# Kernel optimization log

Measured on AMD Instinct MI355X. Metric: run time of the kernel, lower is better.

Reference implementation:

```python
import jax, jax.numpy as jnp
import numpy as np

N = 10000
E = 160000
D_IN = 512
D_OUT = 512


def setup_inputs() -> dict:
    key = jax.random.key(0)
    k1, k2, k3, k4, k5 = jax.random.split(key, 5)
    x = jax.random.normal(k1, (N, D_IN), dtype=jnp.float32)
    edge_index = jax.random.randint(k2, (2, E), 0, N, dtype=jnp.int64)
    edge_attr = jax.random.uniform(k3, (E,), dtype=jnp.float32)
    W = jax.random.normal(k4, (D_IN, D_OUT), dtype=jnp.float32) * 0.05
    b = jax.random.normal(k5, (D_OUT,), dtype=jnp.float32) * 0.05
    return {"x": x, "edge_index": edge_index, "edge_attr": edge_attr, "W": W, "b": b}


def reference(x, edge_index, edge_attr, W, b):
    # PyG GCNConv with normalize=True, add_self_loops=True, edge_weight=edge_attr.
    n = x.shape[0]
    row, col = edge_index[0], edge_index[1]
    # Add self loops with weight 1.0 (fill_value=1.)
    loop = jnp.arange(n, dtype=edge_index.dtype)
    row_f = jnp.concatenate([row, loop])      # [E+N] source nodes
    col_f = jnp.concatenate([col, loop])      # [E+N] target nodes
    ew = jnp.concatenate([edge_attr, jnp.ones((n,), dtype=edge_attr.dtype)])
    # Symmetric normalization: deg computed over target index (col)
    deg = jax.ops.segment_sum(ew, col_f, num_segments=n)
    dinv = jnp.where(deg > 0, jax.lax.rsqrt(deg), 0.0)
    norm = dinv[row_f] * ew * dinv[col_f]     # [E+N]
    # Linear transform (no bias inside lin), then gather-scale-scatter
    h = x @ W                                  # [N, D_OUT]
    msg = h[row_f] * norm[:, None]             # [E+N, D_OUT]
    out = jax.ops.segment_sum(msg, col_f, num_segments=n)
    return out + b
```

## Files before the change

### kernel.cpp

```cpp
#include <hip/hip_runtime.h>

#define NN 10000
#define EE 160000
#define DD 512
#define CAP 128

typedef float floatx4 __attribute__((ext_vector_type(4)));
typedef short short8 __attribute__((ext_vector_type(8)));

#define AS3(p) ((__attribute__((address_space(3))) void*)(p))
#define AS1(p) ((const __attribute__((address_space(1))) void*)(p))

static __device__ __forceinline__ unsigned short f2bf(float f) {
    unsigned int u = __float_as_uint(f);
    unsigned int r = (u + 0x7fffu + ((u >> 16) & 1u)) >> 16;
    return (unsigned short)r;
}
static __device__ __forceinline__ float bflo(unsigned int u) {
    return __uint_as_float(u << 16);
}
static __device__ __forceinline__ float bfhi(unsigned int u) {
    return __uint_as_float(u & 0xffff0000u);
}


#define WT_BLOCKS 256
#define ZERO_BLOCKS 20
#define EDGE_BLOCKS 625
#define GM_BLOCKS (157 * 4)

__global__ __launch_bounds__(256) void k_prep_w(const float* __restrict__ W,
                                                unsigned short* __restrict__ wtb,
                                                uint4* __restrict__ zbase) {
    const int b = blockIdx.x;
    const int tid = threadIdx.x;
    if (b < WT_BLOCKS) {
        __shared__ float T[32][33];
        int bi = b & 15;
        int bj = b >> 4;
        int r0 = tid >> 5;
        int cc = tid & 31;
        #pragma unroll
        for (int k = 0; k < 4; k++) {
            int r = r0 + k * 8;
            T[r][cc] = W[(size_t)(bi * 32 + r) * DD + bj * 32 + cc];
        }
        __syncthreads();
        #pragma unroll
        for (int k = 0; k < 4; k++) {
            int r = r0 + k * 8;
            wtb[(size_t)(bj * 32 + r) * DD + bi * 32 + cc] = f2bf(T[cc][r]);
        }
    } else {
        int idx = (b - WT_BLOCKS) * 256 + tid;
        zbase[idx] = make_uint4(0u, 0u, 0u, 0u);
    }
}


__global__ __launch_bounds__(256) void k_gemm_edge(const float* __restrict__ x,
                                                   const unsigned short* __restrict__ wtb,
                                                   unsigned short* __restrict__ hb,
                                                   const int* __restrict__ row,
                                                   const int* __restrict__ col,
                                                   const float* __restrict__ ew,
                                                   float* __restrict__ deg,
                                                   int* __restrict__ cursor,
                                                   uint2* __restrict__ erw) {
    __shared__ unsigned short As[64 * 32];
    __shared__ unsigned short Bs[128 * 32];

    const int tid = threadIdx.x;

    if (blockIdx.x < EDGE_BLOCKS) {
        int e = blockIdx.x * 256 + tid;
        int r = row[e];
        int t = col[e];
        float w = ew[e];
        atomicAdd(&deg[t], w);
        int p = atomicAdd(&cursor[t], 1);
        if (p < CAP) erw[t * CAP + p] = make_uint2((unsigned int)r, __float_as_uint(w));
        return;
    }

    const int bid = blockIdx.x - EDGE_BLOCKS;
    const int wave = tid >> 6;
    const int lane = tid & 63;

    const int bm = (bid >> 2) * 64;
    const int bn = (bid & 3) * 128;

    const int wm = (wave >> 1) * 32;
    const int wn = (wave & 1) * 64;

    const int fm = lane & 15;
    const int kb = (lane >> 4) * 8;

    floatx4 acc[2][4];
    #pragma unroll
    for (int i = 0; i < 2; i++)
        #pragma unroll
        for (int j = 0; j < 4; j++)
            acc[i][j] = (floatx4){0.f, 0.f, 0.f, 0.f};

    const int srow = lane >> 2;
    const int scol = (lane & 3) * 8;

    int gr = bm + wave * 16 + srow; if (gr > NN - 1) gr = NN - 1;
    const float* xrow = x + (size_t)gr * DD + scol;

    for (int k0 = 0; k0 < DD; k0 += 32) {
        {
            float4 v0 = *(const float4*)(xrow + k0);
            float4 v1 = *(const float4*)(xrow + k0 + 4);
            unsigned int u0 = (unsigned int)f2bf(v0.x) | ((unsigned int)f2bf(v0.y) << 16);
            unsigned int u1 = (unsigned int)f2bf(v0.z) | ((unsigned int)f2bf(v0.w) << 16);
            unsigned int u2 = (unsigned int)f2bf(v1.x) | ((unsigned int)f2bf(v1.y) << 16);
            unsigned int u3 = (unsigned int)f2bf(v1.z) | ((unsigned int)f2bf(v1.w) << 16);
            *(uint4*)&As[(size_t)(wave * 16 + srow) * 32 + scol] = make_uint4(u0, u1, u2, u3);
        }
        #pragma unroll
        for (int cc = 0; cc < 2; cc++) {
            int c = wave + cc * 4;
            int nr = bn + c * 16 + srow;
            __builtin_amdgcn_global_load_lds(AS1(wtb + (size_t)nr * DD + k0 + scol),
                                             AS3(&Bs[c * 512]), 16, 0, 0);
        }
        __syncthreads();

        short8 af[2], bfr[4];
        #pragma unroll
        for (int mi = 0; mi < 2; mi++)
            af[mi] = *(const short8*)&As[(wm + mi * 16 + fm) * 32 + kb];
        #pragma unroll
        for (int ni = 0; ni < 4; ni++)
            bfr[ni] = *(const short8*)&Bs[(wn + ni * 16 + fm) * 32 + kb];

        #pragma unroll
        for (int mi = 0; mi < 2; mi++)
            #pragma unroll
            for (int ni = 0; ni < 4; ni++)
                acc[mi][ni] = __builtin_amdgcn_mfma_f32_16x16x32_bf16(af[mi], bfr[ni], acc[mi][ni], 0, 0, 0);

        __syncthreads();
    }

    #pragma unroll
    for (int mi = 0; mi < 2; mi++) {
        #pragma unroll
        for (int ni = 0; ni < 4; ni++) {
            int colg = bn + wn + ni * 16 + (lane & 15);
            int rbase = bm + wm + mi * 16 + (lane >> 4) * 4;
            #pragma unroll
            for (int j = 0; j < 4; j++) {
                int rg = rbase + j;
                if (rg < NN) hb[(size_t)rg * DD + colg] = f2bf(acc[mi][ni][j]);
            }
        }
    }
}


#define EDGE_FMA(P, W) a0 += bflo(P) * W; a1 += bfhi(P) * W;

__global__ __launch_bounds__(128, 8) void k_aggregate(const int* __restrict__ cursor,
                                                      const uint2* __restrict__ erw,
                                                      const unsigned short* __restrict__ hb,
                                                      const float* __restrict__ deg,
                                                      const float* __restrict__ bias,
                                                      float* __restrict__ out) {
    const int h = threadIdx.x >> 6;
    const int t = threadIdx.x & 63;
    const int bid = blockIdx.x;
    const int q = bid & 3;
    const int i = (bid >> 2) * 2 + h;
    const int c = q * 128 + t * 2;

    __shared__ int   s_r[2][CAP];
    __shared__ float s_w[2][CAP];

    int cnt = cursor[i];
    if (cnt > CAP) cnt = CAP;
    const uint2* bkt = erw + (size_t)i * CAP;
    if (t < cnt) {
        uint2 p = bkt[t];
        int r = (int)p.x;
        s_r[h][t] = r << 9;
        s_w[h][t] = __uint_as_float(p.y) * rsqrtf(deg[r] + 1.0f);
    }
    if (t + 64 < cnt) {
        uint2 p = bkt[t + 64];
        int r = (int)p.x;
        s_r[h][t + 64] = r << 9;
        s_w[h][t + 64] = __uint_as_float(p.y) * rsqrtf(deg[r] + 1.0f);
    }

    float dv = rsqrtf(deg[i] + 1.0f);
    unsigned int hv = *(const unsigned int*)&hb[(size_t)i * DD + c];
    float2 bv = *(const float2*)&bias[c];

    __syncthreads();

    float a0 = 0.f, a1 = 0.f;

    int j = 0;
    for (; j + 8 <= cnt; j += 8) {
        unsigned int p0 = *(const unsigned int*)&hb[s_r[h][j    ] + c];
        unsigned int p1 = *(const unsigned int*)&hb[s_r[h][j + 1] + c];
        unsigned int p2 = *(const unsigned int*)&hb[s_r[h][j + 2] + c];
        unsigned int p3 = *(const unsigned int*)&hb[s_r[h][j + 3] + c];
        unsigned int p4 = *(const unsigned int*)&hb[s_r[h][j + 4] + c];
        unsigned int p5 = *(const unsigned int*)&hb[s_r[h][j + 5] + c];
        unsigned int p6 = *(const unsigned int*)&hb[s_r[h][j + 6] + c];
        unsigned int p7 = *(const unsigned int*)&hb[s_r[h][j + 7] + c];
        float w0 = s_w[h][j],     w1 = s_w[h][j + 1], w2 = s_w[h][j + 2], w3 = s_w[h][j + 3];
        float w4 = s_w[h][j + 4], w5 = s_w[h][j + 5], w6 = s_w[h][j + 6], w7 = s_w[h][j + 7];
        EDGE_FMA(p0, w0) EDGE_FMA(p1, w1) EDGE_FMA(p2, w2) EDGE_FMA(p3, w3)
        EDGE_FMA(p4, w4) EDGE_FMA(p5, w5) EDGE_FMA(p6, w6) EDGE_FMA(p7, w7)
    }
    for (; j + 4 <= cnt; j += 4) {
        unsigned int p0 = *(const unsigned int*)&hb[s_r[h][j    ] + c];
        unsigned int p1 = *(const unsigned int*)&hb[s_r[h][j + 1] + c];
        unsigned int p2 = *(const unsigned int*)&hb[s_r[h][j + 2] + c];
        unsigned int p3 = *(const unsigned int*)&hb[s_r[h][j + 3] + c];
        float w0 = s_w[h][j], w1 = s_w[h][j + 1], w2 = s_w[h][j + 2], w3 = s_w[h][j + 3];
        EDGE_FMA(p0, w0) EDGE_FMA(p1, w1) EDGE_FMA(p2, w2) EDGE_FMA(p3, w3)
    }
    for (; j < cnt; j++) {
        unsigned int p0 = *(const unsigned int*)&hb[s_r[h][j] + c];
        float w0 = s_w[h][j];
        EDGE_FMA(p0, w0)
    }

    float2 o;
    o.x = (a0 + bflo(hv) * dv) * dv + bv.x;
    o.y = (a1 + bfhi(hv) * dv) * dv + bv.y;
    *(float2*)&out[(size_t)i * DD + c] = o;
}

extern "C" void kernel_launch(void* const* d_in, const int* in_sizes, int n_in,
                              void* d_out, int out_size, void* d_ws, size_t ws_size,
                              hipStream_t stream) {
    const float* x  = (const float*)d_in[0];
    const int*   ei = (const int*)d_in[1];
    const float* ea = (const float*)d_in[2];
    const float* W  = (const float*)d_in[3];
    const float* b  = (const float*)d_in[4];
    float* out = (float*)d_out;

    char* ws = (char*)d_ws;
    unsigned short* hb   = (unsigned short*)ws;
    unsigned short* wtb  = (unsigned short*)(ws + 20480000);
    float* deg    = (float*)(ws + 21004288);
    int*   cursor = (int*)  (ws + 21045248);
    uint2* erw    = (uint2*)(ws + 21086208);

    const int* row = ei;
    const int* col = ei + EE;

    k_prep_w<<<WT_BLOCKS + ZERO_BLOCKS, 256, 0, stream>>>(W, wtb, (uint4*)deg);

    k_gemm_edge<<<EDGE_BLOCKS + GM_BLOCKS, 256, 0, stream>>>(x, wtb, hb, row, col, ea,
                                                             deg, cursor, erw);

    k_aggregate<<<NN * 2, 128, 0, stream>>>(cursor, erw, hb, deg, b, out);
}
```

Before: 129.0 us.

## Pre-convert x to bf16 and double-buffer GEMM LDS loads via global_load_lds

Adds a separate pass that converts x to bf16 with a packed convert instruction. The GEMM can then stream both A and B tiles straight into LDS with global_load_lds. The GEMM loop becomes double-buffered with one barrier per k-step, so the next tile loads while the MFMAs run on the current one. Degree and cursor zeroing moves from extra kernel blocks to a hipMemsetAsync. In exchange, the conversion pass writes and re-reads a 10 MB bf16 copy of x and adds a memset call on the stream.

New measurement: 132.0 us. 1.02x slower.

```diff
diff --git a/kernel.cpp b/kernel.cpp
--- a/kernel.cpp
+++ b/kernel.cpp
@@ -16,6 +16,11 @@
     unsigned int r = (u + 0x7fffu + ((u >> 16) & 1u)) >> 16;
     return (unsigned short)r;
 }
+static __device__ __forceinline__ unsigned int cvtpk(float a, float b) {
+    unsigned int r;
+    asm("v_cvt_pk_bf16_f32 %0, %1, %2" : "=v"(r) : "v"(a), "v"(b));
+    return r;
+}
 static __device__ __forceinline__ float bflo(unsigned int u) {
     return __uint_as_float(u << 16);
 }
@@ -24,20 +29,26 @@
 }
 
 
+#define XB_BLOCKS 5000
 #define WT_BLOCKS 256
-#define ZERO_BLOCKS 20
-#define EDGE_BLOCKS 625
+#define EDGE_BLOCKS 632
 #define GM_BLOCKS (157 * 4)
 
-__global__ __launch_bounds__(256) void k_prep_w(const float* __restrict__ W,
-                                                unsigned short* __restrict__ wtb,
-                                                uint4* __restrict__ zbase) {
+__global__ __launch_bounds__(256) void k_prep_xw(const float* __restrict__ x,
+                                                 const float* __restrict__ W,
+                                                 unsigned short* __restrict__ xb,
+                                                 unsigned short* __restrict__ wtb) {
     const int b = blockIdx.x;
     const int tid = threadIdx.x;
-    if (b < WT_BLOCKS) {
+    if (b < XB_BLOCKS) {
+        int gid = b * 256 + tid;
+        float4 v = *(const float4*)&x[(size_t)gid * 4];
+        *(uint2*)&xb[(size_t)gid * 4] = make_uint2(cvtpk(v.x, v.y), cvtpk(v.z, v.w));
+    } else {
         __shared__ float T[32][33];
-        int bi = b & 15;
-        int bj = b >> 4;
+        int idx = b - XB_BLOCKS;
+        int bi = idx & 15;
+        int bj = idx >> 4;
         int r0 = tid >> 5;
         int cc = tid & 31;
         #pragma unroll
@@ -51,14 +62,11 @@
             int r = r0 + k * 8;
             wtb[(size_t)(bj * 32 + r) * DD + bi * 32 + cc] = f2bf(T[cc][r]);
         }
-    } else {
-        int idx = (b - WT_BLOCKS) * 256 + tid;
-        zbase[idx] = make_uint4(0u, 0u, 0u, 0u);
-    }
-}
-
-
-__global__ __launch_bounds__(256) void k_gemm_edge(const float* __restrict__ x,
+    }
+}
+
+
+__global__ __launch_bounds__(256) void k_gemm_edge(const unsigned short* __restrict__ xb,
                                                    const unsigned short* __restrict__ wtb,
                                                    unsigned short* __restrict__ hb,
                                                    const int* __restrict__ row,
@@ -67,19 +75,21 @@
                                                    float* __restrict__ deg,
                                                    int* __restrict__ cursor,
                                                    uint2* __restrict__ erw) {
-    __shared__ unsigned short As[64 * 32];
-    __shared__ unsigned short Bs[128 * 32];
+    __shared__ unsigned short As[2][64 * 32];
+    __shared__ unsigned short Bs[2][128 * 32];
 
     const int tid = threadIdx.x;
 
     if (blockIdx.x < EDGE_BLOCKS) {
         int e = blockIdx.x * 256 + tid;
-        int r = row[e];
-        int t = col[e];
-        float w = ew[e];
-        atomicAdd(&deg[t], w);
-        int p = atomicAdd(&cursor[t], 1);
-        if (p < CAP) erw[t * CAP + p] = make_uint2((unsigned int)r, __float_as_uint(w));
+        if (e < EE) {
+            int r = row[e];
+            int t = col[e];
+            float w = ew[e];
+            atomicAdd(&deg[t], w);
+            int p = atomicAdd(&cursor[t], 1);
+            if (p < CAP) erw[t * CAP + p] = make_uint2((unsigned int)r, __float_as_uint(w));
+        }
         return;
     }
 
@@ -107,43 +117,41 @@
     const int scol = (lane & 3) * 8;
 
     int gr = bm + wave * 16 + srow; if (gr > NN - 1) gr = NN - 1;
-    const float* xrow = x + (size_t)gr * DD + scol;
-
-    for (int k0 = 0; k0 < DD; k0 += 32) {
-        {
-            float4 v0 = *(const float4*)(xrow + k0);
-            float4 v1 = *(const float4*)(xrow + k0 + 4);
-            unsigned int u0 = (unsigned int)f2bf(v0.x) | ((unsigned int)f2bf(v0.y) << 16);
-            unsigned int u1 = (unsigned int)f2bf(v0.z) | ((unsigned int)f2bf(v0.w) << 16);
-            unsigned int u2 = (unsigned int)f2bf(v1.x) | ((unsigned int)f2bf(v1.y) << 16);
-            unsigned int u3 = (unsigned int)f2bf(v1.z) | ((unsigned int)f2bf(v1.w) << 16);
-            *(uint4*)&As[(size_t)(wave * 16 + srow) * 32 + scol] = make_uint4(u0, u1, u2, u3);
-        }
-        #pragma unroll
-        for (int cc = 0; cc < 2; cc++) {
-            int c = wave + cc * 4;
-            int nr = bn + c * 16 + srow;
-            __builtin_amdgcn_global_load_lds(AS1(wtb + (size_t)nr * DD + k0 + scol),
-                                             AS3(&Bs[c * 512]), 16, 0, 0);
-        }
+
+#define STAGE(buf, k0) do {                                                          \
+        __builtin_amdgcn_global_load_lds(AS1(xb + (size_t)gr * DD + (k0) + scol),    \
+                                         AS3(&As[buf][wave * 512]), 16, 0, 0);       \
+        _Pragma("unroll")                                                            \
+        for (int cc = 0; cc < 2; cc++) {                                             \
+            int c = wave + cc * 4;                                                   \
+            int nr = bn + c * 16 + srow;                                             \
+            __builtin_amdgcn_global_load_lds(AS1(wtb + (size_t)nr * DD + (k0) + scol), \
+                                             AS3(&Bs[buf][c * 512]), 16, 0, 0);      \
+        }                                                                            \
+    } while (0)
+
+    STAGE(0, 0);
+
+    for (int k = 0; k < 16; k++) {
+        const int buf = k & 1;
         __syncthreads();
+        if (k < 15) STAGE(buf ^ 1, (k + 1) * 32);
 
         short8 af[2], bfr[4];
         #pragma unroll
         for (int mi = 0; mi < 2; mi++)
-            af[mi] = *(const short8*)&As[(wm + mi * 16 + fm) * 32 + kb];
+            af[mi] = *(const short8*)&As[buf][(wm + mi * 16 + fm) * 32 + kb];
         #pragma unroll
         for (int ni = 0; ni < 4; ni++)
-            bfr[ni] = *(const short8*)&Bs[(wn + ni * 16 + fm) * 32 + kb];
+            bfr[ni] = *(const short8*)&Bs[buf][(wn + ni * 16 + fm) * 32 + kb];
 
         #pragma unroll
         for (int mi = 0; mi < 2; mi++)
             #pragma unroll
             for (int ni = 0; ni < 4; ni++)
                 acc[mi][ni] = __builtin_amdgcn_mfma_f32_16x16x32_bf16(af[mi], bfr[ni], acc[mi][ni], 0, 0, 0);
-
-        __syncthreads();
-    }
+    }
+#undef STAGE
 
     #pragma unroll
     for (int mi = 0; mi < 2; mi++) {
@@ -250,6 +258,7 @@
 
     char* ws = (char*)d_ws;
     unsigned short* hb   = (unsigned short*)ws;
+    unsigned short* xb   = (unsigned short*)(ws + 10240000);
     unsigned short* wtb  = (unsigned short*)(ws + 20480000);
     float* deg    = (float*)(ws + 21004288);
     int*   cursor = (int*)  (ws + 21045248);
@@ -258,9 +267,11 @@
     const int* row = ei;
     const int* col = ei + EE;
 
-    k_prep_w<<<WT_BLOCKS + ZERO_BLOCKS, 256, 0, stream>>>(W, wtb, (uint4*)deg);
-
-    k_gemm_edge<<<EDGE_BLOCKS + GM_BLOCKS, 256, 0, stream>>>(x, wtb, hb, row, col, ea,
+    hipMemsetAsync(deg, 0, 81920, stream);
+
+    k_prep_xw<<<XB_BLOCKS + WT_BLOCKS, 256, 0, stream>>>(x, W, xb, wtb);
+
+    k_gemm_edge<<<EDGE_BLOCKS + GM_BLOCKS, 256, 0, stream>>>(xb, wtb, hb, row, col, ea,
                                                              deg, cursor, erw);
 
     k_aggregate<<<NN * 2, 128, 0, stream>>>(cursor, erw, hb, deg, b, out);
```
